# Kernel tuning notes

Measured on AMD Instinct MI355X. Metric: run time of the kernel, lower is better.

## Reference

```python
import jax, jax.numpy as jnp
import numpy as np

NUM_HEADS = 16
HEAD_DIM = 64
HIDDEN = NUM_HEADS * HEAD_DIM  # 1024
B, T = 32, 512


def setup_inputs() -> dict:
    key = jax.random.key(0)
    ks = jax.random.split(key, 10)
    s = 1.0 / np.sqrt(HIDDEN)
    inp = {
        "x": jax.random.normal(ks[0], (B, HIDDEN, T), dtype=jnp.float32),
        "mask": jax.random.randint(ks[1], (B, T), 0, 2, dtype=jnp.int32),
        "Wq": jax.random.uniform(ks[2], (HIDDEN, HIDDEN), jnp.float32, -s, s),
        "bq": jax.random.uniform(ks[3], (HIDDEN,), jnp.float32, -s, s),
        "Wk": jax.random.uniform(ks[4], (HIDDEN, HIDDEN), jnp.float32, -s, s),
        "bk": jax.random.uniform(ks[5], (HIDDEN,), jnp.float32, -s, s),
        "Wv": jax.random.uniform(ks[6], (HIDDEN, HIDDEN), jnp.float32, -s, s),
        "bv": jax.random.uniform(ks[7], (HIDDEN,), jnp.float32, -s, s),
        "Wo": jax.random.uniform(ks[8], (HIDDEN, HIDDEN), jnp.float32, -s, s),
        "bo": jax.random.uniform(ks[9], (HIDDEN,), jnp.float32, -s, s),
    }
    return inp


def reference(x, mask, Wq, bq, Wk, bk, Wv, bv, Wo, bo):
    # x: [B, hidden, T] -> tokens along last axis
    b, h, t = x.shape
    xt = jnp.swapaxes(x, 1, 2)  # [B, T, hidden]

    def heads(w, bias):
        y = xt @ w.T + bias                       # [B, T, hidden]
        return y.reshape(b, t, NUM_HEADS, HEAD_DIM).transpose(0, 2, 1, 3)  # [B, nh, T, hd]

    q = heads(Wq, bq)
    k = heads(Wk, bk)
    v = heads(Wv, bv)

    scores = jnp.einsum("bhqd,bhkd->bhqk", q, k) / jnp.sqrt(jnp.float32(HEAD_DIM))
    # masked_fill(mask==0, -inf) then clamp to [-50, 50]: masked entries become -50
    scores = jnp.where(mask[:, None, None, :] == 0, -jnp.inf, scores)
    scores = jnp.clip(scores, -50.0, 50.0)
    attn = jax.nn.softmax(scores, axis=-1)        # [B, nh, T, T]
    out = jnp.einsum("bhqk,bhkd->bhqd", attn, v)  # [B, nh, T, hd]
    out = out.transpose(0, 2, 1, 3).reshape(b, t, h)
    out = out @ Wo.T + bo                         # [B, T, hidden]
    return out.max(axis=1)                        # [B, hidden]
```

## Files before the change

kernel.cpp:

```cpp
#include <hip/hip_runtime.h>


typedef _Float16 half8 __attribute__((ext_vector_type(8)));
typedef _Float16 half4 __attribute__((ext_vector_type(4)));
typedef float floatx4 __attribute__((ext_vector_type(4)));
typedef unsigned uintx2 __attribute__((ext_vector_type(2)));

#define HID 1024
#define TT 512
#define NB 32
#define QSCALE 0.1803368801111244f
#define SB2 72.13475204444817f

__device__ __forceinline__ void gload16(const void* g, void* l) {
    __builtin_amdgcn_global_load_lds(
        (const __attribute__((address_space(1))) unsigned int*)g,
        (__attribute__((address_space(3))) unsigned int*)l, 16, 0, 0);
}

__device__ __forceinline__ unsigned fkey(float f) {
    unsigned u = __float_as_uint(f);
    return (u & 0x80000000u) ? ~u : (u | 0x80000000u);
}
__device__ __forceinline__ float funkey(unsigned k) {
    unsigned u = (k & 0x80000000u) ? (k ^ 0x80000000u) : ~k;
    return __uint_as_float(u);
}

__global__ __launch_bounds__(256) void prep_kernel(
    const float* __restrict__ Wq, const float* __restrict__ Wk,
    const float* __restrict__ Wv, const float* __restrict__ Wo,
    _Float16* __restrict__ Wcat,
    const float* __restrict__ x, _Float16* __restrict__ xT,
    unsigned* __restrict__ omax,
    const float* __restrict__ bq, float* __restrict__ bqs)
{
    __shared__ float tile[32][33];
    const int bid = blockIdx.x;
    if (bid < 4096) {
        int i4 = bid * 256 + threadIdx.x;
        int sec = i4 >> 18;
        int off4 = i4 & ((1 << 18) - 1);
        const float* src = (sec == 0) ? Wq : (sec == 1) ? Wk
                          : (sec == 2) ? Wv : Wo;
        float4 v = ((const float4*)src)[off4];
        if (sec == 0) {
            v.x *= QSCALE; v.y *= QSCALE; v.z *= QSCALE; v.w *= QSCALE;
        }
        half4 h = {(_Float16)v.x, (_Float16)v.y, (_Float16)v.z, (_Float16)v.w};
        *(half4*)(Wcat + (size_t)i4 * 4) = h;
    } else if (bid < 20480) {
        int idx = bid - 4096;
        int b = idx >> 9, h0 = ((idx >> 4) & 31) * 32, t0 = (idx & 15) * 32;
        int tx = threadIdx.x & 31, ty = threadIdx.x >> 5;
        const float* xb = x + ((size_t)b * HID + h0) * TT + t0;
        for (int p = 0; p < 4; p++)
            tile[ty + 8 * p][tx] = xb[(ty + 8 * p) * TT + tx];
        __syncthreads();
        if (threadIdx.x < 128) {
            int t = threadIdx.x >> 2, hc = (threadIdx.x & 3) * 8;
            half8 pk;
            for (int k = 0; k < 8; k++)
                pk[k] = (_Float16)tile[hc + k][t];
            *(half8*)(xT + ((size_t)b * TT + t0 + t) * HID + h0 + hc) = pk;
        }
    } else if (bid < 20608) {
        omax[(bid - 20480) * 256 + threadIdx.x] = 0u;
    } else {
        int i = (bid - 20608) * 256 + threadIdx.x;
        bqs[i] = bq[i] * QSCALE;
    }
}

__device__ __forceinline__ void gemm_mainloop(
    const _Float16* __restrict__ Arows,
    const _Float16* __restrict__ Brows,
    _Float16* aT, _Float16* bT, floatx4 acc[4][4], int tid)
{
    const int lane = tid & 63, wid = tid >> 6;
    const int l15 = lane & 15, quad = lane >> 4;
    const int wm = (wid >> 1) * 64, wn = (wid & 1) * 64;

    const int srow = lane >> 3;
    const int sg = (lane & 7) ^ srow;
    const _Float16* ga = Arows + (size_t)(wid * 32 + srow) * 1024 + sg * 8;
    const _Float16* gb = Brows + (size_t)(wid * 32 + srow) * 1024 + sg * 8;
    _Float16* la = aT + wid * 32 * 64;
    _Float16* lb = bT + wid * 32 * 64;

    const int pa = quad ^ (l15 & 7);

    for (int k0 = 0; k0 < 1024; k0 += 64) {
        for (int p = 0; p < 4; p++) {
            gload16(ga + k0 + p * 8 * 1024, la + p * 8 * 64);
            gload16(gb + k0 + p * 8 * 1024, lb + p * 8 * 64);
        }
        __syncthreads();
        for (int kk = 0; kk < 2; kk++) {
            const int pg = kk ? (pa ^ 4) : pa;
            half8 af[4], bf[4];
            for (int mi = 0; mi < 4; mi++)
                af[mi] = *(half8*)(aT + (wm + mi * 16 + l15) * 64 + pg * 8);
            for (int ni = 0; ni < 4; ni++)
                bf[ni] = *(half8*)(bT + (wn + ni * 16 + l15) * 64 + pg * 8);
            for (int mi = 0; mi < 4; mi++)
                for (int ni = 0; ni < 4; ni++)
                    acc[mi][ni] = __builtin_amdgcn_mfma_f32_16x16x32_f16(
                        af[mi], bf[ni], acc[mi][ni], 0, 0, 0);
        }
        __syncthreads();
    }
}

__global__ __launch_bounds__(256) void gemm1_kernel(
    const _Float16* __restrict__ Wcat,
    const float* __restrict__ bqs, const float* __restrict__ bk,
    const float* __restrict__ bv,
    const _Float16* __restrict__ xT,
    _Float16* __restrict__ QT, _Float16* __restrict__ KT,
    _Float16* __restrict__ Vb)
{
    __shared__ __align__(16) char smem[34816];
    _Float16* aT = (_Float16*)smem;
    _Float16* bTl = aT + 128 * 64;

    const int tid = threadIdx.x;
    const int m0 = blockIdx.y * 128, n0 = blockIdx.x * 128, b = blockIdx.z;
    const int lane = tid & 63, wid = tid >> 6;
    const int l15 = lane & 15, quad = lane >> 4;
    const int wm = (wid >> 1) * 64, wn = (wid & 1) * 64;

    floatx4 acc[4][4] = {};
    gemm_mainloop(Wcat + (size_t)m0 * 1024,
                  xT + ((size_t)b * TT + n0) * HID,
                  aT, bTl, acc, tid);

    const int sec = m0 >> 10;
    const int mo = m0 & 1023;

    if (sec < 2) {
        const float* bias = (sec == 0) ? bqs : bk;
        _Float16* dst = (sec == 0) ? QT : KT;
        _Float16* tr = (_Float16*)smem;
        for (int mi = 0; mi < 4; mi++) {
            float bs[4];
            for (int r = 0; r < 4; r++)
                bs[r] = bias[mo + wm + mi * 16 + quad * 4 + r];
            for (int ni = 0; ni < 4; ni++) {
                half4 pk;
                for (int r = 0; r < 4; r++)
                    pk[r] = (_Float16)(acc[mi][ni][r] + bs[r]);
                int tl = wn + ni * 16 + l15;
                int ol = wm + mi * 16 + quad * 4;
                *(half4*)(tr + tl * 136 + ol) = pk;
            }
        }
        __syncthreads();
        int tl = tid >> 1, cb = (tid & 1) * 64;
        for (int ch = 0; ch < 8; ch++) {
            uint4 v = *(uint4*)(tr + tl * 136 + cb + ch * 8);
            *(uint4*)(dst + ((size_t)b * TT + n0 + tl) * HID + mo + cb + ch * 8) = v;
        }
    } else {
        for (int mi = 0; mi < 4; mi++) {
            float bs[4];
            for (int r = 0; r < 4; r++)
                bs[r] = bv[mo + wm + mi * 16 + quad * 4 + r];
            for (int ni = 0; ni < 4; ni++) {
                int t = n0 + wn + ni * 16 + l15;
                for (int r = 0; r < 4; r++) {
                    int o = mo + wm + mi * 16 + quad * 4 + r;
                    Vb[((size_t)b * HID + o) * TT + t] =
                        (_Float16)(acc[mi][ni][r] + bs[r]);
                }
            }
        }
    }
}

__global__ __launch_bounds__(256) void attn_kernel(
    const _Float16* __restrict__ QT, const _Float16* __restrict__ KT,
    const _Float16* __restrict__ Vb, const int* __restrict__ mask,
    _Float16* __restrict__ OcT)
{
    __shared__ __align__(16) _Float16 kvbuf[4 * 4096];
    __shared__ __align__(16) _Float16 ps[2 * 4096];
    __shared__ __align__(16) float msf[2][64];

    const int b = blockIdx.z, hd = blockIdx.y, q0 = blockIdx.x * 128;
    const int tid = threadIdx.x;
    const int lane = tid & 63, wid = tid >> 6;
    const int l15 = lane & 15, quad = lane >> 4;

    const _Float16* QTb = QT + ((size_t)b * TT + q0) * HID + hd * 64;
    const _Float16* KTb = KT + (size_t)b * TT * HID + hd * 64;
    const _Float16* Vbb = Vb + ((size_t)b * HID + hd * 64) * TT;
    const int* mb = mask + b * TT;

    const int srow = lane >> 3;
    const int sg = (lane & 7) ^ srow;
    const int pa = quad ^ (l15 & 7);
    const int pz = l15 & 7;

    for (int qt = 0; qt < 2; qt++)
        for (int p = 0; p < 2; p++) {
            int r = p * 32 + wid * 8 + srow;
            gload16(QTb + (size_t)(qt * 64 + r) * HID + sg * 8,
                    kvbuf + qt * 4096 + (p * 32 + wid * 8) * 64);
        }
    __syncthreads();
    half8 bq[2][2];
    for (int qt = 0; qt < 2; qt++) {
        bq[qt][0] = *(half8*)(kvbuf + qt * 4096 + (wid * 16 + l15) * 64 + pa * 8);
        bq[qt][1] = *(half8*)(kvbuf + qt * 4096 + (wid * 16 + l15) * 64 + (pa ^ 4) * 8);
    }
    __syncthreads();

    auto stage = [&](int jcn, int bufn) {
        int t0n = jcn * 64;
        _Float16* kd = kvbuf + bufn * 4096;
        _Float16* vd = kvbuf + (2 + bufn) * 4096;
        for (int p = 0; p < 2; p++) {
            int r = p * 32 + wid * 8 + srow;
            gload16(KTb + (size_t)(t0n + r) * HID + sg * 8,
                    kd + (p * 32 + wid * 8) * 64);
            gload16(Vbb + (size_t)r * TT + t0n + sg * 8,
                    vd + (p * 32 + wid * 8) * 64);
        }
        if (tid < 64) msf[bufn][tid] = mb[t0n + tid] ? SB2 : -SB2;
    };

    stage(0, 0);

    floatx4 oacc[2][4] = {};
    float rs[2] = {0.f, 0.f};
    const float lo = -SB2;

    for (int jc = 0; jc < 8; jc++) {
        const int cur = jc & 1;
        __syncthreads();
        if (jc < 7) stage(jc + 1, 1 - cur);

        const _Float16* ks = kvbuf + cur * 4096;
        const _Float16* vs = kvbuf + (2 + cur) * 4096;

        for (int jt = 0; jt < 4; jt++) {
            half8 ka0 = *(half8*)(ks + (jt * 16 + l15) * 64 + pa * 8);
            half8 ka1 = *(half8*)(ks + (jt * 16 + l15) * 64 + (pa ^ 4) * 8);
            floatx4 hi = *(floatx4*)(&msf[cur][jt * 16 + quad * 4]);
            for (int qt = 0; qt < 2; qt++) {
                floatx4 sc = {0.f, 0.f, 0.f, 0.f};
                sc = __builtin_amdgcn_mfma_f32_16x16x32_f16(ka0, bq[qt][0], sc, 0, 0, 0);
                sc = __builtin_amdgcn_mfma_f32_16x16x32_f16(ka1, bq[qt][1], sc, 0, 0, 0);
                float e0 = __builtin_amdgcn_exp2f(fminf(fmaxf(sc[0], lo), hi[0]));
                float e1 = __builtin_amdgcn_exp2f(fminf(fmaxf(sc[1], lo), hi[1]));
                float e2 = __builtin_amdgcn_exp2f(fminf(fmaxf(sc[2], lo), hi[2]));
                float e3 = __builtin_amdgcn_exp2f(fminf(fmaxf(sc[3], lo), hi[3]));
                rs[qt] += (e0 + e1) + (e2 + e3);
                unsigned uA = __builtin_bit_cast(
                    unsigned, __builtin_amdgcn_cvt_pkrtz(e0, e1));
                unsigned uB = __builtin_bit_cast(
                    unsigned, __builtin_amdgcn_cvt_pkrtz(e2, e3));
                uintx2 uv = {uA, uB};
                half4 pk = __builtin_bit_cast(half4, uv);
                int g = jt * 2 + (quad >> 1);
                *(half4*)(ps + qt * 4096 + (wid * 16 + l15) * 64 + (g ^ pz) * 8 +
                          (quad & 1) * 4) = pk;
            }
        }
        for (int kc = 0; kc < 2; kc++) {
            int g = kc * 4 + quad;
            half8 bv8[4];
            for (int d4 = 0; d4 < 4; d4++)
                bv8[d4] = *(half8*)(vs + (d4 * 16 + l15) * 64 + (g ^ pz) * 8);
            for (int qt = 0; qt < 2; qt++) {
                half8 ap = *(half8*)(ps + qt * 4096 + (wid * 16 + l15) * 64 +
                                     (g ^ pz) * 8);
                for (int d4 = 0; d4 < 4; d4++)
                    oacc[qt][d4] = __builtin_amdgcn_mfma_f32_16x16x32_f16(
                        ap, bv8[d4], oacc[qt][d4], 0, 0, 0);
            }
        }
    }

    for (int qt = 0; qt < 2; qt++) {
        float s = rs[qt];
        s += __shfl_xor(s, 16, 64);
        s += __shfl_xor(s, 32, 64);
        s = 1.0f / s;
        float inv[4];
        for (int r = 0; r < 4; r++) inv[r] = __shfl(s, quad * 4 + r, 64);
        for (int d4 = 0; d4 < 4; d4++)
            for (int r = 0; r < 4; r++) {
                int t = q0 + qt * 64 + wid * 16 + quad * 4 + r;
                int c = hd * 64 + d4 * 16 + l15;
                OcT[((size_t)b * TT + t) * HID + c] =
                    (_Float16)(oacc[qt][d4][r] * inv[r]);
            }
    }
}

__global__ __launch_bounds__(256) void gemm2_kernel(
    const _Float16* __restrict__ Wo16, const _Float16* __restrict__ OcT,
    unsigned* __restrict__ omax)
{
    __shared__ __align__(16) char smem[2 * 128 * 64 * 2];
    _Float16* aT = (_Float16*)smem;
    _Float16* bTl = aT + 128 * 64;

    const int tid = threadIdx.x;
    const int m0 = blockIdx.y * 128, n0 = blockIdx.x * 128, b = blockIdx.z;
    const int lane = tid & 63, wid = tid >> 6;
    const int l15 = lane & 15, quad = lane >> 4;
    const int wm = (wid >> 1) * 64;

    floatx4 acc[4][4] = {};
    gemm_mainloop(Wo16 + (size_t)m0 * 1024,
                  OcT + ((size_t)b * TT + n0) * HID,
                  aT, bTl, acc, tid);

    for (int mi = 0; mi < 4; mi++)
        for (int r = 0; r < 4; r++) {
            float v = acc[mi][0][r];
            for (int ni = 1; ni < 4; ni++) v = fmaxf(v, acc[mi][ni][r]);
            for (int d = 1; d < 16; d <<= 1) v = fmaxf(v, __shfl_xor(v, d, 64));
            if (l15 == 0) {
                int o = m0 + wm + mi * 16 + quad * 4 + r;
                atomicMax(&omax[b * HID + o], fkey(v));
            }
        }
}

__global__ __launch_bounds__(256) void final_kernel(
    const unsigned* __restrict__ omax, const float* __restrict__ bo,
    float* __restrict__ out)
{
    int i = blockIdx.x * 256 + threadIdx.x;
    out[i] = funkey(omax[i]) + bo[i & 1023];
}

extern "C" void kernel_launch(void* const* d_in, const int* in_sizes, int n_in,
                              void* d_out, int out_size, void* d_ws, size_t ws_size,
                              hipStream_t stream)
{
    const float* x  = (const float*)d_in[0];
    const int* mask = (const int*)d_in[1];
    const float* Wq = (const float*)d_in[2];
    const float* bq = (const float*)d_in[3];
    const float* Wk = (const float*)d_in[4];
    const float* bk = (const float*)d_in[5];
    const float* Wv = (const float*)d_in[6];
    const float* bv = (const float*)d_in[7];
    const float* Wo = (const float*)d_in[8];
    const float* bo = (const float*)d_in[9];
    float* out = (float*)d_out;

    char* ws = (char*)d_ws;
    _Float16* Wcat = (_Float16*)(ws);
    _Float16* xT   = (_Float16*)(ws + (8ull  << 20));
    _Float16* QT   = (_Float16*)(ws + (40ull << 20));
    _Float16* KT   = (_Float16*)(ws + (72ull << 20));
    _Float16* Vb   = (_Float16*)(ws + (104ull << 20));
    _Float16* OcT  = (_Float16*)(ws + (136ull << 20));
    unsigned* omax = (unsigned*)(ws + (168ull << 20));
    float*    bqs  = (float*)(ws + (168ull << 20) + (128ull << 10));

    prep_kernel<<<20612, 256, 0, stream>>>(Wq, Wk, Wv, Wo, Wcat, x, xT, omax,
                                           bq, bqs);
    gemm1_kernel<<<dim3(4, 24, 32), 256, 0, stream>>>(Wcat, bqs, bk, bv, xT, QT, KT, Vb);
    attn_kernel<<<dim3(4, 16, 32), 256, 0, stream>>>(QT, KT, Vb, mask, OcT);
    gemm2_kernel<<<dim3(4, 8, 32), 256, 0, stream>>>(Wcat + (3ull << 20), OcT, omax);
    final_kernel<<<128, 256, 0, stream>>>(omax, bo, out);
}
```

Before: 360.3 us.

## Remap blocks per XCD for L2 locality and widen x transpose tiles

Converts the 3D grids of gemm1, attention and gemm2 to 1D grids and remaps block IDs so that blocks sharing the same batch/column tile (or batch/head) land on the same XCD. The goal is to reuse the shared B operand or K/V in that XCD's L2 instead of fetching it from memory. The prep transpose also moves to 64x64 tiles with float4 loads, and every thread now writes two output rows, which cuts the block count. The larger padded tile raises LDS use and may bring some bank conflicts on the scalar tile stores.

```diff
diff --git a/kernel.cpp b/kernel.cpp
--- a/kernel.cpp
+++ b/kernel.cpp
@@ -35,7 +35,7 @@
     unsigned* __restrict__ omax,
     const float* __restrict__ bq, float* __restrict__ bqs)
 {
-    __shared__ float tile[32][33];
+    __shared__ float tile[64][65];
     const int bid = blockIdx.x;
     if (bid < 4096) {
         int i4 = bid * 256 + threadIdx.x;
@@ -49,25 +49,32 @@
         }
         half4 h = {(_Float16)v.x, (_Float16)v.y, (_Float16)v.z, (_Float16)v.w};
         *(half4*)(Wcat + (size_t)i4 * 4) = h;
-    } else if (bid < 20480) {
+    } else if (bid < 8192) {
         int idx = bid - 4096;
-        int b = idx >> 9, h0 = ((idx >> 4) & 31) * 32, t0 = (idx & 15) * 32;
-        int tx = threadIdx.x & 31, ty = threadIdx.x >> 5;
+        int b = idx >> 7, h0 = ((idx >> 3) & 15) * 64, t0 = (idx & 7) * 64;
+        int tx = threadIdx.x & 15, ty = threadIdx.x >> 4;
         const float* xb = x + ((size_t)b * HID + h0) * TT + t0;
-        for (int p = 0; p < 4; p++)
-            tile[ty + 8 * p][tx] = xb[(ty + 8 * p) * TT + tx];
-        __syncthreads();
-        if (threadIdx.x < 128) {
-            int t = threadIdx.x >> 2, hc = (threadIdx.x & 3) * 8;
+        for (int p = 0; p < 4; p++) {
+            int r = ty + 16 * p;
+            float4 v = *(const float4*)(xb + (size_t)r * TT + tx * 4);
+            tile[r][tx * 4 + 0] = v.x;
+            tile[r][tx * 4 + 1] = v.y;
+            tile[r][tx * 4 + 2] = v.z;
+            tile[r][tx * 4 + 3] = v.w;
+        }
+        __syncthreads();
+        int hc = (threadIdx.x & 7) * 8, tb = threadIdx.x >> 3;
+        for (int rd = 0; rd < 2; rd++) {
+            int tt = tb + 32 * rd;
             half8 pk;
             for (int k = 0; k < 8; k++)
-                pk[k] = (_Float16)tile[hc + k][t];
-            *(half8*)(xT + ((size_t)b * TT + t0 + t) * HID + h0 + hc) = pk;
-        }
-    } else if (bid < 20608) {
-        omax[(bid - 20480) * 256 + threadIdx.x] = 0u;
+                pk[k] = (_Float16)tile[hc + k][tt];
+            *(half8*)(xT + ((size_t)b * TT + t0 + tt) * HID + h0 + hc) = pk;
+        }
+    } else if (bid < 8320) {
+        omax[(bid - 8192) * 256 + threadIdx.x] = 0u;
     } else {
-        int i = (bid - 20608) * 256 + threadIdx.x;
+        int i = (bid - 8320) * 256 + threadIdx.x;
         bqs[i] = bq[i] * QSCALE;
     }
 }
@@ -125,7 +132,12 @@
     _Float16* bTl = aT + 128 * 64;
 
     const int tid = threadIdx.x;
-    const int m0 = blockIdx.y * 128, n0 = blockIdx.x * 128, b = blockIdx.z;
+    const int id = blockIdx.x;
+    const int xcd = id & 7, slot = id >> 3;
+    const int grp = xcd + 8 * (slot / 24);
+    const int m0 = (slot % 24) * 128;
+    const int n0 = (grp & 3) * 128;
+    const int b = grp >> 2;
     const int lane = tid & 63, wid = tid >> 6;
     const int l15 = lane & 15, quad = lane >> 4;
     const int wm = (wid >> 1) * 64, wn = (wid & 1) * 64;
@@ -187,7 +199,11 @@
     __shared__ __align__(16) _Float16 ps[2 * 4096];
     __shared__ __align__(16) float msf[2][64];
 
-    const int b = blockIdx.z, hd = blockIdx.y, q0 = blockIdx.x * 128;
+    const int id = blockIdx.x;
+    const int xcd = id & 7, slot = id >> 3;
+    const int grp = xcd + 8 * (slot >> 2);
+    const int q0 = (slot & 3) * 128;
+    const int hd = grp & 15, b = grp >> 4;
     const int tid = threadIdx.x;
     const int lane = tid & 63, wid = tid >> 6;
     const int l15 = lane & 15, quad = lane >> 4;
@@ -309,7 +325,12 @@
     _Float16* bTl = aT + 128 * 64;
 
     const int tid = threadIdx.x;
-    const int m0 = blockIdx.y * 128, n0 = blockIdx.x * 128, b = blockIdx.z;
+    const int id = blockIdx.x;
+    const int xcd = id & 7, slot = id >> 3;
+    const int grp = xcd + 8 * (slot >> 3);
+    const int m0 = (slot & 7) * 128;
+    const int n0 = (grp & 3) * 128;
+    const int b = grp >> 2;
     const int lane = tid & 63, wid = tid >> 6;
     const int l15 = lane & 15, quad = lane >> 4;
     const int wm = (wid >> 1) * 64;
@@ -365,10 +386,10 @@
     unsigned* omax = (unsigned*)(ws + (168ull << 20));
     float*    bqs  = (float*)(ws + (168ull << 20) + (128ull << 10));
 
-    prep_kernel<<<20612, 256, 0, stream>>>(Wq, Wk, Wv, Wo, Wcat, x, xT, omax,
-                                           bq, bqs);
-    gemm1_kernel<<<dim3(4, 24, 32), 256, 0, stream>>>(Wcat, bqs, bk, bv, xT, QT, KT, Vb);
-    attn_kernel<<<dim3(4, 16, 32), 256, 0, stream>>>(QT, KT, Vb, mask, OcT);
-    gemm2_kernel<<<dim3(4, 8, 32), 256, 0, stream>>>(Wcat + (3ull << 20), OcT, omax);
+    prep_kernel<<<8324, 256, 0, stream>>>(Wq, Wk, Wv, Wo, Wcat, x, xT, omax,
+                                          bq, bqs);
+    gemm1_kernel<<<3072, 256, 0, stream>>>(Wcat, bqs, bk, bv, xT, QT, KT, Vb);
+    attn_kernel<<<2048, 256, 0, stream>>>(QT, KT, Vb, mask, OcT);
+    gemm2_kernel<<<1024, 256, 0, stream>>>(Wcat + (3ull << 20), OcT, omax);
     final_kernel<<<128, 256, 0, stream>>>(omax, bo, out);
 }
```

Result: faster. 349.1 us (-3.1%).
